# Performance work log

Hardware: AMD Instinct MI355X
Metric: run time of the kernel (lower is better)

## Reference

```python
import jax, jax.numpy as jnp
import numpy as np

B, S, M, D, H = 2, 2048, 512, 1024, 16
HD = D // H      # head dim 64
KVC = D // 16    # MLA kv compression dim 64
QC = D // 32     # MLA q compression dim 32
RD = HD          # retrieval (qk) head dim 64
LOOKBACK = 8     # cross_window
EPS = 1e-6


def rmsnorm(x, w):
    return x * jax.lax.rsqrt(jnp.mean(x * x, axis=-1, keepdims=True) + EPS) * w


def setup_inputs():
    key = jax.random.key(0)
    ks = jax.random.split(key, 20)
    g = lambda i, shape: jax.random.normal(ks[i], shape, jnp.float32) * 0.02
    return {
        "x": jax.random.normal(ks[0], (B, S, D), jnp.float32),
        "memory": jax.random.normal(ks[1], (B, M, D), jnp.float32),
        "seg_ids": jnp.sort(jax.random.randint(ks[2], (B, S), 0, M), axis=-1),
        "norm1_w": jnp.ones((D,), jnp.float32),
        "W_dq": g(3, (D, QC)),
        "W_uq": g(4, (QC, H * RD)),
        "W_dkv": g(5, (D, KVC)),
        "W_uk": g(6, (KVC, H * RD)),
        "W_uv": g(7, (KVC, H * HD)),
        "W_o_self": g(8, (H * HD, D)),
        "norm2_w": jnp.ones((D,), jnp.float32),
        "W_q_c": g(9, (D, D)),
        "W_k_c": g(10, (D, D)),
        "W_v_c": g(11, (D, D)),
        "W_o_c": g(12, (D, D)),
        "norm3_w": jnp.ones((D,), jnp.float32),
        "W_gate": g(13, (D, 4 * D)),
        "W_up": g(14, (D, 4 * D)),
        "W_down": g(15, (4 * D, D)),
    }


def reference(x, memory, seg_ids, norm1_w, W_dq, W_uq, W_dkv, W_uk, W_uv,
              W_o_self, norm2_w, W_q_c, W_k_c, W_v_c, W_o_c, norm3_w,
              W_gate, W_up, W_down):
    # ---- MLA causal self-attention (low-rank compressed q/kv) ----
    h = rmsnorm(x, norm1_w)
    q = ((h @ W_dq) @ W_uq).reshape(B, S, H, RD)
    c_kv = h @ W_dkv                                  # [B,S,KVC]
    k = (c_kv @ W_uk).reshape(B, S, H, RD)
    v = (c_kv @ W_uv).reshape(B, S, H, HD)
    scores = jnp.einsum('bihd,bjhd->bhij', q, k) / np.float32(np.sqrt(RD))
    causal = jnp.tril(jnp.ones((S, S), bool))
    scores = jnp.where(causal, scores, -jnp.inf)
    attn = jax.nn.softmax(scores, axis=-1)
    o = jnp.einsum('bhij,bjhd->bihd', attn, v).reshape(B, S, H * HD)
    x = x + o @ W_o_self
    # ---- segment sliding-window cross-attention ----
    h = rmsnorm(x, norm2_w)
    qc = (h @ W_q_c).reshape(B, S, H, HD)
    kc = (memory @ W_k_c).reshape(B, M, H, HD)
    vc = (memory @ W_v_c).reshape(B, M, H, HD)
    sc = jnp.einsum('bihd,bjhd->bhij', qc, kc) / np.float32(np.sqrt(HD))
    kv_pos = jnp.arange(M)
    seg = seg_ids[:, :, None]                          # [B,S,1]
    allowed = (kv_pos[None, None, :] <= seg) & (kv_pos[None, None, :] >= seg - LOOKBACK)
    sc = jnp.where(allowed[:, None, :, :], sc, -jnp.inf)
    ac = jax.nn.softmax(sc, axis=-1)
    oc = jnp.einsum('bhij,bjhd->bihd', ac, vc).reshape(B, S, D)
    x = x + oc @ W_o_c
    # ---- SwiGLU FFN ----
    h = rmsnorm(x, norm3_w)
    x = x + (jax.nn.silu(h @ W_gate) * (h @ W_up)) @ W_down
    return x
```

## Files before the change

### kernel.cpp

```cpp
#include <hip/hip_runtime.h>
#include <stdint.h>

typedef unsigned short U16;
typedef __bf16 bf16x8 __attribute__((ext_vector_type(8)));
typedef unsigned short us8 __attribute__((ext_vector_type(8)));
typedef float f32x4 __attribute__((ext_vector_type(4)));

__device__ __forceinline__ U16 f2bf(float f) {
    unsigned u = __builtin_bit_cast(unsigned, f);
    unsigned r = (u + 0x7fff + ((u >> 16) & 1)) >> 16;
    return (U16)r;
}
__device__ __forceinline__ U16 f2bf_fast(float f) {
    return (U16)((__builtin_bit_cast(unsigned, f) + 0x8000u) >> 16);
}
__device__ __forceinline__ float bf2f(U16 v) {
    return __builtin_bit_cast(float, (unsigned)v << 16);
}
__device__ __forceinline__ bf16x8 ld8(const U16* p) { return __builtin_bit_cast(bf16x8, *(const us8*)p); }

__device__ __forceinline__ void async16(const U16* g, U16* l) {
    auto* gp = (const __attribute__((address_space(1))) U16*)g;
    auto* lp = (__attribute__((address_space(3))) U16*)(uintptr_t)(uint32_t)(uintptr_t)l;
    __builtin_amdgcn_global_load_lds(gp, lp, 16, 0, 0);
}

struct WEnt { const float* src; U16* dst; int K, N, Kpad, Npad, koff, noff, tiles; };
struct WTable { WEnt e[13]; };

__global__ __launch_bounds__(256) void wtrans_all(WTable t) {
    int bx = blockIdx.x, ei = 0;
    while (bx >= t.e[ei].tiles) { bx -= t.e[ei].tiles; ei++; }
    const WEnt E = t.e[ei];
    const int ntn = E.Npad >> 5;
    const int n0 = (bx % ntn) * 32, k0 = (bx / ntn) * 32;
    __shared__ float tile[32][33];
    const int tx = threadIdx.x & 31, ty = threadIdx.x >> 5;
#pragma unroll
    for (int i = 0; i < 4; i++) {
        int kk = k0 + ty + i * 8, n = n0 + tx;
        int k = kk - E.koff;
        float v = (k >= 0 && k < E.K && n < E.N) ? E.src[(size_t)k * E.N + n] : 0.f;
        tile[ty + i * 8][tx] = v;
    }
    __syncthreads();
#pragma unroll
    for (int i = 0; i < 4; i++) {
        int n = n0 + ty + i * 8, kk = k0 + tx;
        E.dst[(size_t)(E.noff + n) * E.Kpad + kk] = f2bf(tile[tx][ty + i * 8]);
    }
}

__global__ __launch_bounds__(256) void f2bf_k(const float* __restrict__ in, U16* __restrict__ out, int n) {
    int i = (blockIdx.x * 256 + threadIdx.x) * 4;
    if (i < n) {
        float4 v = *(const float4*)(in + i);
        out[i + 0] = f2bf(v.x); out[i + 1] = f2bf(v.y);
        out[i + 2] = f2bf(v.z); out[i + 3] = f2bf(v.w);
    }
}

__global__ __launch_bounds__(256) void rmsnorm_k(const float* __restrict__ x, const float* __restrict__ w,
                                                 U16* __restrict__ h) {
    const int row = blockIdx.x, tid = threadIdx.x;
    const float4 v = *(const float4*)(x + (size_t)row * 1024 + tid * 4);
    float ss = v.x * v.x + v.y * v.y + v.z * v.z + v.w * v.w;
#pragma unroll
    for (int o = 32; o > 0; o >>= 1) ss += __shfl_xor(ss, o);
    __shared__ float red[4];
    if ((tid & 63) == 0) red[tid >> 6] = ss;
    __syncthreads();
    float tot = red[0] + red[1] + red[2] + red[3];
    float sc = rsqrtf(tot * (1.0f / 1024.0f) + 1e-6f);
    const float4 wv = *(const float4*)(w + tid * 4);
    U16* hp = h + (size_t)row * 1024 + tid * 4;
    hp[0] = f2bf(v.x * sc * wv.x); hp[1] = f2bf(v.y * sc * wv.y);
    hp[2] = f2bf(v.z * sc * wv.z); hp[3] = f2bf(v.w * sc * wv.w);
}

template <int EPI>
__global__ __launch_bounds__(256) void gemm2(const U16* __restrict__ A, const U16* __restrict__ Bt,
                                             void* __restrict__ Cout, const float* __restrict__ resid,
                                             int M, int N, int K, int lda, int ldb, int ldc) {
    __shared__ __align__(16) U16 As[2][128 * 32];
    __shared__ __align__(16) U16 Bs[2][128 * 32];
    const int tid = threadIdx.x;
    const int m0 = blockIdx.y * 128, n0 = blockIdx.x * 128;
    const int k0 = blockIdx.z * K;
    const int wave = tid >> 6, lane = tid & 63, l16 = lane & 15, quad = lane >> 4;
    const int wm = (wave >> 1) * 64, wn = (wave & 1) * 64;
    const int sr = lane >> 2, sc = (lane & 3) * 8;
    const U16* gA = A + (size_t)(m0 + wave * 32 + sr) * lda + sc + k0;
    const U16* gB = Bt + (size_t)(n0 + wave * 32 + sr) * ldb + sc + k0;
    f32x4 acc[4][4] = {};
    for (int kt = 0; kt < K; kt += 64) {
        __syncthreads();
#pragma unroll
        for (int p = 0; p < 2; p++) {
            const int o = kt + p * 32;
            async16(gA + o, &As[p][(wave * 32) * 32]);
            async16(gA + (size_t)16 * lda + o, &As[p][(wave * 32 + 16) * 32]);
            async16(gB + o, &Bs[p][(wave * 32) * 32]);
            async16(gB + (size_t)16 * ldb + o, &Bs[p][(wave * 32 + 16) * 32]);
        }
        __syncthreads();
#pragma unroll
        for (int p = 0; p < 2; p++) {
            bf16x8 af[4], bfr[4];
#pragma unroll
            for (int i = 0; i < 4; i++) {
                af[i]  = ld8(&As[p][(wm + i * 16 + l16) * 32 + quad * 8]);
                bfr[i] = ld8(&Bs[p][(wn + i * 16 + l16) * 32 + quad * 8]);
            }
#pragma unroll
            for (int mi = 0; mi < 4; mi++)
#pragma unroll
                for (int ni = 0; ni < 4; ni++)
                    acc[mi][ni] = __builtin_amdgcn_mfma_f32_16x16x32_bf16(af[mi], bfr[ni], acc[mi][ni], 0, 0, 0);
        }
    }
    if constexpr (EPI == 2) {
        __shared__ __align__(16) U16 Ts[4][64 * 80];
        U16* T = Ts[wave];
#pragma unroll
        for (int mi = 0; mi < 4; mi++)
#pragma unroll
            for (int ni = 0; ni < 4; ni++)
#pragma unroll
                for (int r = 0; r < 4; r++)
                    T[(ni * 16 + l16) * 80 + mi * 16 + quad * 4 + r] = f2bf(acc[mi][ni][r]);
#pragma unroll
        for (int c = 0; c < 8; c++) {
            int nloc = (lane >> 3) + 8 * c, mloc = (lane & 7) * 8;
            us8 v = *(const us8*)&T[nloc * 80 + mloc];
            *(us8*)&((U16*)Cout)[(size_t)(n0 + wn + nloc) * ldc + (m0 + wm + mloc)] = v;
        }
    } else {
#pragma unroll
        for (int mi = 0; mi < 4; mi++) {
#pragma unroll
            for (int r = 0; r < 4; r++) {
                int m = m0 + wm + mi * 16 + quad * 4 + r;
#pragma unroll
                for (int ni = 0; ni < 4; ni++) {
                    int n = n0 + wn + ni * 16 + l16;
                    float val = acc[mi][ni][r];
                    if (EPI == 0) ((U16*)Cout)[(size_t)m * ldc + n] = f2bf(val);
                    else if (EPI == 4) {
                        if (blockIdx.z == 0) val += resid[(size_t)m * ldc + n];
                        atomicAdd(&((float*)Cout)[(size_t)m * ldc + n], val);
                    }
                }
            }
        }
    }
}

template <int EPI>
__global__ __launch_bounds__(256) void gemm_m64(const U16* __restrict__ A, const U16* __restrict__ Bt,
                                                void* __restrict__ Cout, const float* __restrict__ resid,
                                                int M, int N, int K, int lda, int ldb, int ldc) {
    __shared__ __align__(16) U16 As[4][64 * 32];
    __shared__ __align__(16) U16 Bs[4][128 * 32];
    const int tid = threadIdx.x;
    const int m0 = blockIdx.y * 64, n0 = blockIdx.x * 128;
    const int k0 = blockIdx.z * K;
    const int wave = tid >> 6, lane = tid & 63, l16 = lane & 15, quad = lane >> 4;
    const int wm = (wave >> 1) * 32, wn = (wave & 1) * 64;
    const int sr = lane >> 2, sc = (lane & 3) * 8;
    const U16* gA = A + (size_t)(m0 + wave * 16 + sr) * lda + sc + k0;
    const U16* gB = Bt + (size_t)(n0 + wave * 32 + sr) * ldb + sc + k0;
    f32x4 acc[2][4] = {};
    for (int kt = 0; kt < K; kt += 128) {
        __syncthreads();
#pragma unroll
        for (int p = 0; p < 4; p++) {
            const int o = kt + p * 32;
            async16(gA + o, &As[p][(wave * 16) * 32]);
            async16(gB + o, &Bs[p][(wave * 32) * 32]);
            async16(gB + (size_t)16 * ldb + o, &Bs[p][(wave * 32 + 16) * 32]);
        }
        __syncthreads();
#pragma unroll
        for (int p = 0; p < 4; p++) {
            bf16x8 af[2], bfr[4];
#pragma unroll
            for (int i = 0; i < 2; i++)
                af[i] = ld8(&As[p][(wm + i * 16 + l16) * 32 + quad * 8]);
#pragma unroll
            for (int i = 0; i < 4; i++)
                bfr[i] = ld8(&Bs[p][(wn + i * 16 + l16) * 32 + quad * 8]);
#pragma unroll
            for (int mi = 0; mi < 2; mi++)
#pragma unroll
                for (int ni = 0; ni < 4; ni++)
                    acc[mi][ni] = __builtin_amdgcn_mfma_f32_16x16x32_bf16(af[mi], bfr[ni], acc[mi][ni], 0, 0, 0);
        }
    }
#pragma unroll
    for (int mi = 0; mi < 2; mi++) {
#pragma unroll
        for (int r = 0; r < 4; r++) {
            int m = m0 + wm + mi * 16 + quad * 4 + r;
#pragma unroll
            for (int ni = 0; ni < 4; ni++) {
                int n = n0 + wn + ni * 16 + l16;
                float val = acc[mi][ni][r];
                if (EPI == 0) ((U16*)Cout)[(size_t)m * ldc + n] = f2bf(val);
                else if (EPI == 1) ((float*)Cout)[(size_t)m * ldc + n] = resid[(size_t)m * ldc + n] + val;
                else if (EPI == 3) atomicAdd(&((float*)Cout)[(size_t)m * ldc + n], val);
            }
        }
    }
}

__global__ __launch_bounds__(256) void ffn1_fused(const U16* __restrict__ A, const U16* __restrict__ Wgu,
                                                  U16* __restrict__ Cout) {
    __shared__ __align__(16) U16 As[2][128 * 32];
    __shared__ __align__(16) U16 Gs[2][64 * 32];
    __shared__ __align__(16) U16 Us[2][64 * 32];
    const int tid = threadIdx.x;
    const int m0 = blockIdx.y * 128, n0 = blockIdx.x * 64;
    const int wave = tid >> 6, lane = tid & 63, l16 = lane & 15, quad = lane >> 4;
    const int wm = (wave >> 1) * 64, wn = (wave & 1) * 32;
    const int sr = lane >> 2, sc = (lane & 3) * 8;
    const U16* gA = A + (size_t)(m0 + wave * 32 + sr) * 1024 + sc;
    const U16* gG = Wgu + (size_t)(n0 + wave * 16 + sr) * 1024 + sc;
    const U16* gU = gG + (size_t)4096 * 1024;
    f32x4 ag[4][2] = {}, au[4][2] = {};
    for (int kt = 0; kt < 1024; kt += 64) {
        __syncthreads();
#pragma unroll
        for (int p = 0; p < 2; p++) {
            const int o = kt + p * 32;
            async16(gA + o, &As[p][(wave * 32) * 32]);
            async16(gA + 16 * 1024 + o, &As[p][(wave * 32 + 16) * 32]);
            async16(gG + o, &Gs[p][(wave * 16) * 32]);
            async16(gU + o, &Us[p][(wave * 16) * 32]);
        }
        __syncthreads();
#pragma unroll
        for (int p = 0; p < 2; p++) {
            bf16x8 af[4], bg[2], bu[2];
#pragma unroll
            for (int i = 0; i < 4; i++)
                af[i] = ld8(&As[p][(wm + i * 16 + l16) * 32 + quad * 8]);
#pragma unroll
            for (int i = 0; i < 2; i++) {
                bg[i] = ld8(&Gs[p][(wn + i * 16 + l16) * 32 + quad * 8]);
                bu[i] = ld8(&Us[p][(wn + i * 16 + l16) * 32 + quad * 8]);
            }
#pragma unroll
            for (int mi = 0; mi < 4; mi++)
#pragma unroll
                for (int ni = 0; ni < 2; ni++) {
                    ag[mi][ni] = __builtin_amdgcn_mfma_f32_16x16x32_bf16(af[mi], bg[ni], ag[mi][ni], 0, 0, 0);
                    au[mi][ni] = __builtin_amdgcn_mfma_f32_16x16x32_bf16(af[mi], bu[ni], au[mi][ni], 0, 0, 0);
                }
        }
    }
#pragma unroll
    for (int mi = 0; mi < 4; mi++) {
#pragma unroll
        for (int r = 0; r < 4; r++) {
            int m = m0 + wm + mi * 16 + quad * 4 + r;
#pragma unroll
            for (int ni = 0; ni < 2; ni++) {
                int n = n0 + wn + ni * 16 + l16;
                float g = ag[mi][ni][r], u = au[mi][ni][r];
                float act = g / (1.f + __expf(-g)) * u;
                Cout[(size_t)m * 4096 + n] = f2bf(act);
            }
        }
    }
}

__global__ __launch_bounds__(256) void flash_self3(const U16* __restrict__ QK, const U16* __restrict__ Vt,
                                                   U16* __restrict__ Og) {
    __shared__ __align__(16) U16 Ps[4 * 1280];
    __shared__ float Ored[4 * 2080];
    __shared__ float Lred[128];
    const int wave = threadIdx.x >> 6, lane = threadIdx.x & 63;
    const int l16 = lane & 15, quad = lane >> 4;
    const int bx = blockIdx.x;
    const int t = 63 - (bx >> 5);
    const int bh = bx & 31, b = bh >> 4, h = bh & 15;
    const int q0 = t * 32;
    const size_t rowQ0 = (size_t)(b * 2048 + q0 + l16) * 2048 + h * 64;
    const size_t rowQ1 = rowQ0 + 16 * 2048;
    bf16x8 aq[2][2];
    aq[0][0] = ld8(QK + rowQ0 + quad * 8);  aq[0][1] = ld8(QK + rowQ0 + 32 + quad * 8);
    aq[1][0] = ld8(QK + rowQ1 + quad * 8);  aq[1][1] = ld8(QK + rowQ1 + 32 + quad * 8);
    const U16* Kbase = QK + (size_t)(b * 2048) * 2048 + 1024 + h * 64;
    const U16* Vbase = Vt + (size_t)(h * 64) * 4096 + b * 2048;
    f32x4 o[2][4] = {};
    float ls[2][4] = {};
    U16* Pw = &Ps[wave * 1280];
    const int prd = l16 * 40 + ((quad ^ (l16 >> 2)) << 3);
    const int jend = q0 + 32;
    for (int j0 = wave * 32; j0 < jend; j0 += 128) {
        const U16* kp = Kbase + (size_t)j0 * 2048;
        bf16x8 b00 = ld8(kp + (size_t)l16 * 2048 + quad * 8);
        bf16x8 b01 = ld8(kp + (size_t)l16 * 2048 + 32 + quad * 8);
        bf16x8 b10 = ld8(kp + (size_t)(16 + l16) * 2048 + quad * 8);
        bf16x8 b11 = ld8(kp + (size_t)(16 + l16) * 2048 + 32 + quad * 8);
        bf16x8 v0 = ld8(Vbase + (size_t)(0  + l16) * 4096 + j0 + quad * 8);
        bf16x8 v1 = ld8(Vbase + (size_t)(16 + l16) * 4096 + j0 + quad * 8);
        bf16x8 v2 = ld8(Vbase + (size_t)(32 + l16) * 4096 + j0 + quad * 8);
        bf16x8 v3 = ld8(Vbase + (size_t)(48 + l16) * 4096 + j0 + quad * 8);
        f32x4 s[2][2] = {};
#pragma unroll
        for (int g = 0; g < 2; g++) {
            s[g][0] = __builtin_amdgcn_mfma_f32_16x16x32_bf16(aq[g][0], b00, s[g][0], 0, 0, 0);
            s[g][0] = __builtin_amdgcn_mfma_f32_16x16x32_bf16(aq[g][1], b01, s[g][0], 0, 0, 0);
            s[g][1] = __builtin_amdgcn_mfma_f32_16x16x32_bf16(aq[g][0], b10, s[g][1], 0, 0, 0);
            s[g][1] = __builtin_amdgcn_mfma_f32_16x16x32_bf16(aq[g][1], b11, s[g][1], 0, 0, 0);
        }
        float p0[2][4], p1[2][4];
        if (j0 + 32 >= jend) {
#pragma unroll
            for (int g = 0; g < 2; g++)
#pragma unroll
                for (int r = 0; r < 4; r++) {
                    int qg = q0 + g * 16 + quad * 4 + r;
                    p0[g][r] = (j0 + l16 <= qg) ? __expf(fminf(s[g][0][r] * 0.125f, 30.f)) : 0.f;
                    p1[g][r] = (j0 + 16 + l16 <= qg) ? __expf(fminf(s[g][1][r] * 0.125f, 30.f)) : 0.f;
                }
        } else {
#pragma unroll
            for (int g = 0; g < 2; g++)
#pragma unroll
                for (int r = 0; r < 4; r++) {
                    p0[g][r] = __expf(fminf(s[g][0][r] * 0.125f, 30.f));
                    p1[g][r] = __expf(fminf(s[g][1][r] * 0.125f, 30.f));
                }
        }
#pragma unroll
        for (int g = 0; g < 2; g++)
#pragma unroll
            for (int r = 0; r < 4; r++) {
                ls[g][r] += p0[g][r] + p1[g][r];
                int row = quad * 4 + r;
                Pw[g * 640 + row * 40 + ((((l16 >> 3) + 0) ^ quad) << 3) + (l16 & 7)] = f2bf_fast(p0[g][r]);
                Pw[g * 640 + row * 40 + ((((l16 >> 3) + 2) ^ quad) << 3) + (l16 & 7)] = f2bf_fast(p1[g][r]);
            }
#pragma unroll
        for (int g = 0; g < 2; g++) {
            bf16x8 ap = ld8(&Pw[g * 640 + prd]);
            o[g][0] = __builtin_amdgcn_mfma_f32_16x16x32_bf16(ap, v0, o[g][0], 0, 0, 0);
            o[g][1] = __builtin_amdgcn_mfma_f32_16x16x32_bf16(ap, v1, o[g][1], 0, 0, 0);
            o[g][2] = __builtin_amdgcn_mfma_f32_16x16x32_bf16(ap, v2, o[g][2], 0, 0, 0);
            o[g][3] = __builtin_amdgcn_mfma_f32_16x16x32_bf16(ap, v3, o[g][3], 0, 0, 0);
        }
    }
    float* Or = &Ored[wave * 2080];
#pragma unroll
    for (int g = 0; g < 2; g++) {
#pragma unroll
        for (int dg = 0; dg < 4; dg++)
#pragma unroll
            for (int r = 0; r < 4; r++)
                Or[(g * 16 + quad * 4 + r) * 65 + dg * 16 + l16] = o[g][dg][r];
#pragma unroll
        for (int r = 0; r < 4; r++) {
            float v = ls[g][r];
            v += __shfl_xor(v, 1); v += __shfl_xor(v, 2);
            v += __shfl_xor(v, 4); v += __shfl_xor(v, 8);
            if (l16 == 0) Lred[wave * 32 + g * 16 + quad * 4 + r] = v;
        }
    }
    __syncthreads();
    const int q = threadIdx.x >> 3, d0 = (threadIdx.x & 7) * 8;
    float l = Lred[q] + Lred[32 + q] + Lred[64 + q] + Lred[96 + q];
    float inv = 1.0f / l;
    us8 outv;
#pragma unroll
    for (int i = 0; i < 8; i++) {
        int idx = q * 65 + d0 + i;
        float s = Ored[idx] + Ored[2080 + idx] + Ored[4160 + idx] + Ored[6240 + idx];
        outv[i] = f2bf(s * inv);
    }
    *(us8*)(Og + (size_t)(b * 2048 + q0 + q) * 1024 + h * 64 + d0) = outv;
}

__global__ __launch_bounds__(256) void cross_attn(const U16* __restrict__ qc, const U16* __restrict__ kvc,
                                                  const int* __restrict__ seg_ids, U16* __restrict__ oc) {
    const int tok = blockIdx.x;
    const int b = tok >> 11;
    const int w = threadIdx.x >> 6, lane = threadIdx.x & 63;
    const int h = blockIdx.y * 4 + w;
    const int seg = seg_ids[tok];
    const size_t qoff = (size_t)tok * 1024 + h * 64 + lane;
    float q = bf2f(qc[qoff]);
    float s[9];
#pragma unroll
    for (int jj = 0; jj < 9; jj++) {
        int j = seg - 8 + jj;
        float sc = -INFINITY;
        if (j >= 0) {
            float kv = bf2f(kvc[((size_t)(b * 512) + j) * 2048 + h * 64 + lane]);
            sc = q * kv;
            sc += __shfl_xor(sc, 1); sc += __shfl_xor(sc, 2); sc += __shfl_xor(sc, 4);
            sc += __shfl_xor(sc, 8); sc += __shfl_xor(sc, 16); sc += __shfl_xor(sc, 32);
            sc *= 0.125f;
        }
        s[jj] = sc;
    }
    float m = s[0];
#pragma unroll
    for (int jj = 1; jj < 9; jj++) m = fmaxf(m, s[jj]);
    float l = 0.f, o = 0.f;
#pragma unroll
    for (int jj = 0; jj < 9; jj++) {
        int j = seg - 8 + jj;
        if (j >= 0) {
            float p = __expf(s[jj] - m);
            l += p;
            o += p * bf2f(kvc[((size_t)(b * 512) + j) * 2048 + 1024 + h * 64 + lane]);
        }
    }
    oc[qoff] = f2bf(o / l);
}

extern "C" void kernel_launch(void* const* d_in, const int* in_sizes, int n_in,
                              void* d_out, int out_size, void* d_ws, size_t ws_size,
                              hipStream_t stream) {
    const float* x      = (const float*)d_in[0];
    const float* memory = (const float*)d_in[1];
    const int*   seg    = (const int*)d_in[2];
    const float* n1w    = (const float*)d_in[3];
    const float* W_dq   = (const float*)d_in[4];
    const float* W_uq   = (const float*)d_in[5];
    const float* W_dkv  = (const float*)d_in[6];
    const float* W_uk   = (const float*)d_in[7];
    const float* W_uv   = (const float*)d_in[8];
    const float* W_os   = (const float*)d_in[9];
    const float* n2w    = (const float*)d_in[10];
    const float* W_qc   = (const float*)d_in[11];
    const float* W_kc   = (const float*)d_in[12];
    const float* W_vc   = (const float*)d_in[13];
    const float* W_oc   = (const float*)d_in[14];
    const float* n3w    = (const float*)d_in[15];
    const float* W_gate = (const float*)d_in[16];
    const float* W_up   = (const float*)d_in[17];
    const float* W_down = (const float*)d_in[18];
    (void)in_sizes; (void)n_in; (void)out_size; (void)ws_size;

    char* ws = (char*)d_ws;
    size_t off = 0;
    auto alloc = [&](size_t bytes) -> void* {
        void* p = ws + off;
        off += (bytes + 255) & ~(size_t)255;
        return p;
    };
    const size_t MB = 1024 * 1024;
    U16* hbuf     = (U16*)alloc(8 * MB);
    float* x1     = (float*)alloc(16 * MB);
    float* x2     = (float*)alloc(16 * MB);
    float* cq32   = (float*)alloc(2 * MB);
    U16* Wt_dqkv  = (U16*)alloc(128 * 1024 * 2);
    U16* Wt_uqk   = (U16*)alloc(2048 * 128 * 2);
    U16* Wt_uv    = (U16*)alloc(1024 * 128 * 2);
    U16* Wt_os    = (U16*)alloc(1024 * 1024 * 2);
    U16* Wt_qc    = (U16*)alloc(1024 * 1024 * 2);
    U16* Wt_kvc   = (U16*)alloc((size_t)2048 * 1024 * 2);
    U16* Wt_oc    = (U16*)alloc(1024 * 1024 * 2);
    U16* Wt_gu    = (U16*)alloc((size_t)8192 * 1024 * 2);
    U16* Wt_down  = (U16*)alloc((size_t)1024 * 4096 * 2);
    U16* mem_bf   = (U16*)alloc(1024 * 1024 * 2);
    char* arena   = ws + off;
    U16* cq  = (U16*)(arena);
    U16* qkb = (U16*)(arena + 1 * MB);
    U16* vt  = (U16*)(arena + 17 * MB);
    U16* ob  = (U16*)(arena + 25 * MB);
    U16* qcb  = (U16*)(arena);
    U16* kvcb = (U16*)(arena + 8 * MB);
    U16* ocb  = (U16*)(arena + 12 * MB);
    U16* gact = (U16*)(arena);

    WTable T;
    int i = 0;
    auto ent = [&](const float* s, U16* d, int K, int N, int Kpad, int Npad, int koff, int noff) {
        T.e[i++] = WEnt{s, d, K, N, Kpad, Npad, koff, noff, (Kpad >> 5) * (Npad >> 5)};
    };
    ent(W_dq,   Wt_dqkv, 1024, 32,   1024, 32,   0,  0);
    ent(W_dkv,  Wt_dqkv, 1024, 64,   1024, 96,   0,  32);
    ent(W_uq,   Wt_uqk,  32,   1024, 128,  1024, 0,  0);
    ent(W_uk,   Wt_uqk,  64,   1024, 128,  1024, 32, 1024);
    ent(W_uv,   Wt_uv,   64,   1024, 128,  1024, 32, 0);
    ent(W_os,   Wt_os,   1024, 1024, 1024, 1024, 0,  0);
    ent(W_qc,   Wt_qc,   1024, 1024, 1024, 1024, 0,  0);
    ent(W_kc,   Wt_kvc,  1024, 1024, 1024, 1024, 0,  0);
    ent(W_vc,   Wt_kvc,  1024, 1024, 1024, 1024, 0,  1024);
    ent(W_oc,   Wt_oc,   1024, 1024, 1024, 1024, 0,  0);
    ent(W_gate, Wt_gu,   1024, 4096, 1024, 4096, 0,  0);
    ent(W_up,   Wt_gu,   1024, 4096, 1024, 4096, 0,  4096);
    ent(W_down, Wt_down, 4096, 1024, 4096, 1024, 0,  0);
    int total_tiles = 0;
    for (int j = 0; j < 13; j++) total_tiles += T.e[j].tiles;
    wtrans_all<<<total_tiles, 256, 0, stream>>>(T);
    f2bf_k<<<1024, 256, 0, stream>>>(memory, mem_bf, 1024 * 1024);
    hipMemsetAsync(cq32, 0, (size_t)4096 * 128 * 4, stream);
    hipMemsetAsync(d_out, 0, (size_t)4096 * 1024 * 4, stream);

    rmsnorm_k<<<4096, 256, 0, stream>>>(x, n1w, hbuf);
    gemm_m64<3><<<dim3(1, 64, 4), 256, 0, stream>>>(hbuf, Wt_dqkv, cq32, nullptr, 4096, 128, 256, 1024, 1024, 128);
    f2bf_k<<<512, 256, 0, stream>>>(cq32, cq, 4096 * 128);
    gemm2<0><<<dim3(16, 32), 256, 0, stream>>>(cq, Wt_uqk, qkb, nullptr, 4096, 2048, 128, 128, 128, 2048);
    gemm2<2><<<dim3(8, 32),  256, 0, stream>>>(cq, Wt_uv,  vt,  nullptr, 4096, 1024, 128, 128, 128, 4096);
    flash_self3<<<2048, 256, 0, stream>>>(qkb, vt, ob);
    gemm_m64<1><<<dim3(8, 64), 256, 0, stream>>>(ob, Wt_os, x1, x, 4096, 1024, 1024, 1024, 1024, 1024);

    rmsnorm_k<<<4096, 256, 0, stream>>>(x1, n2w, hbuf);
    gemm_m64<0><<<dim3(8, 64),  256, 0, stream>>>(hbuf,   Wt_qc,  qcb,  nullptr, 4096, 1024, 1024, 1024, 1024, 1024);
    gemm_m64<0><<<dim3(16, 16), 256, 0, stream>>>(mem_bf, Wt_kvc, kvcb, nullptr, 1024, 2048, 1024, 1024, 1024, 2048);
    cross_attn<<<dim3(4096, 4), 256, 0, stream>>>(qcb, kvcb, seg, ocb);
    gemm_m64<1><<<dim3(8, 64),  256, 0, stream>>>(ocb,    Wt_oc,  x2,   x1,      4096, 1024, 1024, 1024, 1024, 1024);

    rmsnorm_k<<<4096, 256, 0, stream>>>(x2, n3w, hbuf);
    ffn1_fused<<<dim3(64, 32), 256, 0, stream>>>(hbuf, Wt_gu, gact);
    gemm2<4><<<dim3(8, 32, 2), 256, 0, stream>>>(gact, Wt_down, (float*)d_out, x2, 4096, 1024, 2048, 4096, 4096, 1024);
}
```

Baseline: 580.1 us.

## Merge small GEMM launches and replace atomic split-K with partial-buffer reduction

Replaces the atomic split-K down-projection and compressed-q projection with plain stores: split-K partials are written to separate buffers and summed by a new reduce kernel, and the FFN down GEMM now runs as a single non-split gemm_m64 with a fused residual. The up-q/k and up-v GEMMs are merged into one launch that dispatches by block index, and likewise the cross-attention q and memory k/v projections. This removes two memsets, the atomics and several launches. In exchange it adds an extra partial buffer, and the down GEMM does longer K loops per block with less parallelism than the split-K version.

Result: faster. 526.4 us (-9.3%).

```diff
diff --git a/kernel.cpp b/kernel.cpp
--- a/kernel.cpp
+++ b/kernel.cpp
@@ -58,6 +58,18 @@
         out[i + 0] = f2bf(v.x); out[i + 1] = f2bf(v.y);
         out[i + 2] = f2bf(v.z); out[i + 3] = f2bf(v.w);
     }
+}
+
+__global__ __launch_bounds__(256) void cq_reduce(const float* __restrict__ p, U16* __restrict__ out) {
+    int i = (blockIdx.x * 256 + threadIdx.x) * 4;
+    const float4 a = *(const float4*)(p + i);
+    const float4 b = *(const float4*)(p + 524288 + i);
+    const float4 c = *(const float4*)(p + 2 * 524288 + i);
+    const float4 d = *(const float4*)(p + 3 * 524288 + i);
+    out[i + 0] = f2bf(a.x + b.x + c.x + d.x);
+    out[i + 1] = f2bf(a.y + b.y + c.y + d.y);
+    out[i + 2] = f2bf(a.z + b.z + c.z + d.z);
+    out[i + 3] = f2bf(a.w + b.w + c.w + d.w);
 }
 
 __global__ __launch_bounds__(256) void rmsnorm_k(const float* __restrict__ x, const float* __restrict__ w,
@@ -78,30 +90,32 @@
     hp[2] = f2bf(v.z * sc * wv.z); hp[3] = f2bf(v.w * sc * wv.w);
 }
 
-template <int EPI>
-__global__ __launch_bounds__(256) void gemm2(const U16* __restrict__ A, const U16* __restrict__ Bt,
-                                             void* __restrict__ Cout, const float* __restrict__ resid,
-                                             int M, int N, int K, int lda, int ldb, int ldc) {
+__global__ __launch_bounds__(256) void qkuv_gemm(const U16* __restrict__ A, const U16* __restrict__ Wuqk,
+                                                 const U16* __restrict__ Wuv,
+                                                 U16* __restrict__ qkb, U16* __restrict__ vt) {
     __shared__ __align__(16) U16 As[2][128 * 32];
     __shared__ __align__(16) U16 Bs[2][128 * 32];
+    __shared__ __align__(16) U16 Ts[4][64 * 80];
     const int tid = threadIdx.x;
-    const int m0 = blockIdx.y * 128, n0 = blockIdx.x * 128;
-    const int k0 = blockIdx.z * K;
+    const bool isuv = blockIdx.x >= 16;
+    const U16* Bt = isuv ? Wuv : Wuqk;
+    const int n0 = (isuv ? blockIdx.x - 16 : blockIdx.x) * 128;
+    const int m0 = blockIdx.y * 128;
     const int wave = tid >> 6, lane = tid & 63, l16 = lane & 15, quad = lane >> 4;
     const int wm = (wave >> 1) * 64, wn = (wave & 1) * 64;
     const int sr = lane >> 2, sc = (lane & 3) * 8;
-    const U16* gA = A + (size_t)(m0 + wave * 32 + sr) * lda + sc + k0;
-    const U16* gB = Bt + (size_t)(n0 + wave * 32 + sr) * ldb + sc + k0;
+    const U16* gA = A + (size_t)(m0 + wave * 32 + sr) * 128 + sc;
+    const U16* gB = Bt + (size_t)(n0 + wave * 32 + sr) * 128 + sc;
     f32x4 acc[4][4] = {};
-    for (int kt = 0; kt < K; kt += 64) {
+    for (int kt = 0; kt < 128; kt += 64) {
         __syncthreads();
 #pragma unroll
         for (int p = 0; p < 2; p++) {
             const int o = kt + p * 32;
             async16(gA + o, &As[p][(wave * 32) * 32]);
-            async16(gA + (size_t)16 * lda + o, &As[p][(wave * 32 + 16) * 32]);
+            async16(gA + 16 * 128 + o, &As[p][(wave * 32 + 16) * 32]);
             async16(gB + o, &Bs[p][(wave * 32) * 32]);
-            async16(gB + (size_t)16 * ldb + o, &Bs[p][(wave * 32 + 16) * 32]);
+            async16(gB + 16 * 128 + o, &Bs[p][(wave * 32 + 16) * 32]);
         }
         __syncthreads();
 #pragma unroll
@@ -119,8 +133,7 @@
                     acc[mi][ni] = __builtin_amdgcn_mfma_f32_16x16x32_bf16(af[mi], bfr[ni], acc[mi][ni], 0, 0, 0);
         }
     }
-    if constexpr (EPI == 2) {
-        __shared__ __align__(16) U16 Ts[4][64 * 80];
+    if (isuv) {
         U16* T = Ts[wave];
 #pragma unroll
         for (int mi = 0; mi < 4; mi++)
@@ -133,26 +146,18 @@
         for (int c = 0; c < 8; c++) {
             int nloc = (lane >> 3) + 8 * c, mloc = (lane & 7) * 8;
             us8 v = *(const us8*)&T[nloc * 80 + mloc];
-            *(us8*)&((U16*)Cout)[(size_t)(n0 + wn + nloc) * ldc + (m0 + wm + mloc)] = v;
+            *(us8*)&vt[(size_t)(n0 + wn + nloc) * 4096 + (m0 + wm + mloc)] = v;
         }
     } else {
 #pragma unroll
-        for (int mi = 0; mi < 4; mi++) {
+        for (int mi = 0; mi < 4; mi++)
 #pragma unroll
             for (int r = 0; r < 4; r++) {
                 int m = m0 + wm + mi * 16 + quad * 4 + r;
 #pragma unroll
-                for (int ni = 0; ni < 4; ni++) {
-                    int n = n0 + wn + ni * 16 + l16;
-                    float val = acc[mi][ni][r];
-                    if (EPI == 0) ((U16*)Cout)[(size_t)m * ldc + n] = f2bf(val);
-                    else if (EPI == 4) {
-                        if (blockIdx.z == 0) val += resid[(size_t)m * ldc + n];
-                        atomicAdd(&((float*)Cout)[(size_t)m * ldc + n], val);
-                    }
-                }
+                for (int ni = 0; ni < 4; ni++)
+                    qkb[(size_t)m * 2048 + n0 + wn + ni * 16 + l16] = f2bf(acc[mi][ni][r]);
             }
-        }
     }
 }
 
@@ -208,10 +213,62 @@
                 float val = acc[mi][ni][r];
                 if (EPI == 0) ((U16*)Cout)[(size_t)m * ldc + n] = f2bf(val);
                 else if (EPI == 1) ((float*)Cout)[(size_t)m * ldc + n] = resid[(size_t)m * ldc + n] + val;
-                else if (EPI == 3) atomicAdd(&((float*)Cout)[(size_t)m * ldc + n], val);
+                else if (EPI == 5) ((float*)Cout)[(size_t)blockIdx.z * 524288 + (size_t)m * ldc + n] = val;
             }
         }
     }
+}
+
+__global__ __launch_bounds__(256) void qckv_gemm(const U16* __restrict__ hbuf, const U16* __restrict__ Wqc,
+                                                 const U16* __restrict__ memb, const U16* __restrict__ Wkvc,
+                                                 U16* __restrict__ qcb, U16* __restrict__ kvcb) {
+    __shared__ __align__(16) U16 As[4][64 * 32];
+    __shared__ __align__(16) U16 Bs[4][128 * 32];
+    const int tid = threadIdx.x, bid = blockIdx.x;
+    const U16 *A, *Bt; U16* C; int m0, n0, ldc;
+    if (bid < 512) { A = hbuf; Bt = Wqc;  C = qcb;  m0 = (bid >> 3) * 64; n0 = (bid & 7) * 128;  ldc = 1024; }
+    else { int b2 = bid - 512; A = memb; Bt = Wkvc; C = kvcb; m0 = (b2 >> 4) * 64; n0 = (b2 & 15) * 128; ldc = 2048; }
+    const int wave = tid >> 6, lane = tid & 63, l16 = lane & 15, quad = lane >> 4;
+    const int wm = (wave >> 1) * 32, wn = (wave & 1) * 64;
+    const int sr = lane >> 2, sc = (lane & 3) * 8;
+    const U16* gA = A + (size_t)(m0 + wave * 16 + sr) * 1024 + sc;
+    const U16* gB = Bt + (size_t)(n0 + wave * 32 + sr) * 1024 + sc;
+    f32x4 acc[2][4] = {};
+    for (int kt = 0; kt < 1024; kt += 128) {
+        __syncthreads();
+#pragma unroll
+        for (int p = 0; p < 4; p++) {
+            const int o = kt + p * 32;
+            async16(gA + o, &As[p][(wave * 16) * 32]);
+            async16(gB + o, &Bs[p][(wave * 32) * 32]);
+            async16(gB + 16 * 1024 + o, &Bs[p][(wave * 32 + 16) * 32]);
+        }
+        __syncthreads();
+#pragma unroll
+        for (int p = 0; p < 4; p++) {
+            bf16x8 af[2], bfr[4];
+#pragma unroll
+            for (int i = 0; i < 2; i++)
+                af[i] = ld8(&As[p][(wm + i * 16 + l16) * 32 + quad * 8]);
+#pragma unroll
+            for (int i = 0; i < 4; i++)
+                bfr[i] = ld8(&Bs[p][(wn + i * 16 + l16) * 32 + quad * 8]);
+#pragma unroll
+            for (int mi = 0; mi < 2; mi++)
+#pragma unroll
+                for (int ni = 0; ni < 4; ni++)
+                    acc[mi][ni] = __builtin_amdgcn_mfma_f32_16x16x32_bf16(af[mi], bfr[ni], acc[mi][ni], 0, 0, 0);
+        }
+    }
+#pragma unroll
+    for (int mi = 0; mi < 2; mi++)
+#pragma unroll
+        for (int r = 0; r < 4; r++) {
+            int m = m0 + wm + mi * 16 + quad * 4 + r;
+#pragma unroll
+            for (int ni = 0; ni < 4; ni++)
+                C[(size_t)m * ldc + n0 + wn + ni * 16 + l16] = f2bf(acc[mi][ni][r]);
+        }
 }
 
 __global__ __launch_bounds__(256) void ffn1_fused(const U16* __restrict__ A, const U16* __restrict__ Wgu,
@@ -457,7 +514,7 @@
     U16* hbuf     = (U16*)alloc(8 * MB);
     float* x1     = (float*)alloc(16 * MB);
     float* x2     = (float*)alloc(16 * MB);
-    float* cq32   = (float*)alloc(2 * MB);
+    float* cq32   = (float*)alloc(8 * MB);
     U16* Wt_dqkv  = (U16*)alloc(128 * 1024 * 2);
     U16* Wt_uqk   = (U16*)alloc(2048 * 128 * 2);
     U16* Wt_uv    = (U16*)alloc(1024 * 128 * 2);
@@ -500,24 +557,20 @@
     for (int j = 0; j < 13; j++) total_tiles += T.e[j].tiles;
     wtrans_all<<<total_tiles, 256, 0, stream>>>(T);
     f2bf_k<<<1024, 256, 0, stream>>>(memory, mem_bf, 1024 * 1024);
-    hipMemsetAsync(cq32, 0, (size_t)4096 * 128 * 4, stream);
-    hipMemsetAsync(d_out, 0, (size_t)4096 * 1024 * 4, stream);
 
     rmsnorm_k<<<4096, 256, 0, stream>>>(x, n1w, hbuf);
-    gemm_m64<3><<<dim3(1, 64, 4), 256, 0, stream>>>(hbuf, Wt_dqkv, cq32, nullptr, 4096, 128, 256, 1024, 1024, 128);
-    f2bf_k<<<512, 256, 0, stream>>>(cq32, cq, 4096 * 128);
-    gemm2<0><<<dim3(16, 32), 256, 0, stream>>>(cq, Wt_uqk, qkb, nullptr, 4096, 2048, 128, 128, 128, 2048);
-    gemm2<2><<<dim3(8, 32),  256, 0, stream>>>(cq, Wt_uv,  vt,  nullptr, 4096, 1024, 128, 128, 128, 4096);
+    gemm_m64<5><<<dim3(1, 64, 4), 256, 0, stream>>>(hbuf, Wt_dqkv, cq32, nullptr, 4096, 128, 256, 1024, 1024, 128);
+    cq_reduce<<<512, 256, 0, stream>>>(cq32, cq);
+    qkuv_gemm<<<dim3(24, 32), 256, 0, stream>>>(cq, Wt_uqk, Wt_uv, qkb, vt);
     flash_self3<<<2048, 256, 0, stream>>>(qkb, vt, ob);
     gemm_m64<1><<<dim3(8, 64), 256, 0, stream>>>(ob, Wt_os, x1, x, 4096, 1024, 1024, 1024, 1024, 1024);
 
     rmsnorm_k<<<4096, 256, 0, stream>>>(x1, n2w, hbuf);
-    gemm_m64<0><<<dim3(8, 64),  256, 0, stream>>>(hbuf,   Wt_qc,  qcb,  nullptr, 4096, 1024, 1024, 1024, 1024, 1024);
-    gemm_m64<0><<<dim3(16, 16), 256, 0, stream>>>(mem_bf, Wt_kvc, kvcb, nullptr, 1024, 2048, 1024, 1024, 1024, 2048);
+    qckv_gemm<<<768, 256, 0, stream>>>(hbuf, Wt_qc, mem_bf, Wt_kvc, qcb, kvcb);
     cross_attn<<<dim3(4096, 4), 256, 0, stream>>>(qcb, kvcb, seg, ocb);
-    gemm_m64<1><<<dim3(8, 64),  256, 0, stream>>>(ocb,    Wt_oc,  x2,   x1,      4096, 1024, 1024, 1024, 1024, 1024);
+    gemm_m64<1><<<dim3(8, 64), 256, 0, stream>>>(ocb, Wt_oc, x2, x1, 4096, 1024, 1024, 1024, 1024, 1024);
 
     rmsnorm_k<<<4096, 256, 0, stream>>>(x2, n3w, hbuf);
     ffn1_fused<<<dim3(64, 32), 256, 0, stream>>>(hbuf, Wt_gu, gact);
-    gemm2<4><<<dim3(8, 32, 2), 256, 0, stream>>>(gact, Wt_down, (float*)d_out, x2, 4096, 1024, 2048, 4096, 4096, 1024);
-}
+    gemm_m64<1><<<dim3(8, 64), 256, 0, stream>>>(gact, Wt_down, (float*)d_out, x2, 4096, 1024, 4096, 4096, 4096, 1024);
+}
```
